# Kernel tuning notes

Hardware: AMD Instinct MI355X
Metric: run time of the kernel (lower is better)

## Reference

```python
import jax, jax.numpy as jnp
import numpy as np

L2 = 65536          # edges per orientation (L=256 torus)
N = 2 * L2          # total edges
FIN = 8             # nfeatCNN_in
FOUT = 8            # nfeatCNN_out
K = 13              # kernel size (neighbor shifts per edge)
SCALE = (2.0 + 2.0 * np.e) / (np.e - 1.0)


def setup_inputs() -> dict:
    key = jax.random.key(0)
    ks = jax.random.split(key, 8)
    x = jax.random.normal(ks[0], (FIN * N,), dtype=jnp.float32)
    Wconv_hor = jax.random.normal(ks[1], (FOUT, FIN, K), dtype=jnp.float32) * 0.1
    Wconv_vert = jax.random.normal(ks[2], (FOUT, FIN, K), dtype=jnp.float32) * 0.1
    bconv_hor = jnp.zeros((FOUT,), dtype=jnp.float32)
    bconv_vert = jnp.zeros((FOUT,), dtype=jnp.float32)
    mask_hor = jax.random.randint(ks[3], (L2, FOUT, FIN, K), 0, 2).astype(bool)
    mask_vert = jax.random.randint(ks[4], (L2, FOUT, FIN, K), 0, 2).astype(bool)
    ker_hor = jax.random.randint(ks[5], (L2, K), 0, N, dtype=jnp.int32)
    ker_vert = jax.random.randint(ks[6], (L2, K), 0, N, dtype=jnp.int32)
    hor_edge_lst = jnp.arange(L2, dtype=jnp.int32)
    vert_edge_lst = jnp.arange(L2, dtype=jnp.int32) + L2
    return {
        "x": x,
        "Wconv_hor": Wconv_hor, "Wconv_vert": Wconv_vert,
        "bconv_hor": bconv_hor, "bconv_vert": bconv_vert,
        "mask_hor": mask_hor, "mask_vert": mask_vert,
        "ker_hor": ker_hor, "ker_vert": ker_vert,
        "hor_edge_lst": hor_edge_lst, "vert_edge_lst": vert_edge_lst,
    }


def reference(x, Wconv_hor, Wconv_vert, bconv_hor, bconv_vert,
              mask_hor, mask_vert, ker_hor, ker_vert,
              hor_edge_lst, vert_edge_lst):
    fout, fin, _ = Wconv_hor.shape
    n = x.shape[0] // fin
    xm = x.reshape(fin, n)                      # (fin, N)

    def branch(W, mask, ker, b):
        xg = xm[:, ker]                         # gather -> (fin, E, K)
        Wm = W[None] * mask.astype(W.dtype)     # (E, fout, fin, K)
        # per-edge masked contraction over (fin, K); vectorized over edges
        z = jnp.einsum('eoik,iek->oe', Wm, xg)  # (fout, E)
        return z + b[:, None]

    x_hor = branch(Wconv_hor, mask_hor, ker_hor, bconv_hor)
    x_vert = branch(Wconv_vert, mask_vert, ker_vert, bconv_vert)

    out = jnp.zeros((fout, n), dtype=x.dtype)
    out = out.at[:, hor_edge_lst].set(x_hor)
    out = out.at[:, vert_edge_lst].set(x_vert)
    return (jax.nn.sigmoid(out) - 0.5) * jnp.asarray(SCALE, out.dtype)
```

## Files before the change

### kernel.cpp

```cpp
#include <hip/hip_runtime.h>
#include <math.h>

#define L2C   65536
#define NC    (2 * L2C)
#define FINC  8
#define FOUTC 8
#define KC    13
#define BLOCK 256
#define EPB   4
#define EWORDS (FOUTC * FINC * KC)

constexpr double E_D = 2.71828182845904523536;
constexpr float SCALE_F = (float)((2.0 + 2.0 * E_D) / (E_D - 1.0));


__global__ __launch_bounds__(256)
void transpose_x_kernel(const float* __restrict__ x, float* __restrict__ xt) {
    int n = blockIdx.x * 256 + threadIdx.x;
    float v[FINC];
#pragma unroll
    for (int i = 0; i < FINC; ++i) v[i] = x[(size_t)i * NC + n];
    float4* dst = reinterpret_cast<float4*>(xt + ((size_t)n << 3));
    dst[0] = make_float4(v[0], v[1], v[2], v[3]);
    dst[1] = make_float4(v[4], v[5], v[6], v[7]);
}

__global__ __launch_bounds__(BLOCK)
void edge_conv_kernel(const float* __restrict__ xt,
                      const float* __restrict__ Wh, const float* __restrict__ Wv,
                      const float* __restrict__ bh, const float* __restrict__ bv,
                      const unsigned char* __restrict__ mh,
                      const unsigned char* __restrict__ mv,
                      const int* __restrict__ kh, const int* __restrict__ kv,
                      float* __restrict__ out)
{
    __shared__ float        Wsh[EWORDS];
    __shared__ unsigned int msh[EPB * EWORDS];

    const int tid  = threadIdx.x;
    const int lane = tid & 63;
    const int wave = tid >> 6;
    const int o    = lane >> 3;
    const int i    = lane & 7;

    const int blk = blockIdx.x;
    const int blocks_per_branch = L2C / EPB;
    const bool hor = (blk < blocks_per_branch);

    const float*         W    = hor ? Wh  : Wv;
    const float*         bias = hor ? bh  : bv;
    const unsigned char* mask = hor ? mh  : mv;
    const int*           ker  = hor ? kh  : kv;
    const int bblk = hor ? blk : blk - blocks_per_branch;
    const int be   = bblk * EPB + wave;
    const int col  = hor ? be : (be + L2C);

    int cols[KC];
#pragma unroll
    for (int k = 0; k < KC; ++k) cols[k] = ker[(size_t)be * KC + k];

    const unsigned char probe = mh[(size_t)(lane * 4 + 1)];
    const bool words = (__ballot(probe != 0) == 0ull);

    if (words) {
        const uint4* g4 = reinterpret_cast<const uint4*>(
            mask + (size_t)bblk * (EPB * EWORDS * 4));
        uint4* m4 = reinterpret_cast<uint4*>(msh);
#pragma unroll
        for (int idx = tid; idx < EPB * EWORDS / 4; idx += BLOCK)
            m4[idx] = g4[idx];
    } else {
        const uint4* g4 = reinterpret_cast<const uint4*>(
            mask + (size_t)bblk * (EPB * EWORDS));
        uint4* m4 = reinterpret_cast<uint4*>(msh);
        if (tid < EPB * EWORDS / 16)
            m4[tid] = g4[tid];
    }

    if (tid < EWORDS / 4)
        reinterpret_cast<float4*>(Wsh)[tid] = reinterpret_cast<const float4*>(W)[tid];

    __syncthreads();

    float acc0 = 0.0f, acc1 = 0.0f;
    if (words) {
        const unsigned int* mrow = msh + wave * EWORDS + lane * KC;
#pragma unroll
        for (int k = 0; k < KC; ++k) {
            const float xv = xt[((size_t)cols[k] << 3) + i];
            const float wk = Wsh[lane * KC + k];
            const float wm = mrow[k] ? wk : 0.0f;
            if (k & 1) acc1 = fmaf(wm, xv, acc1);
            else       acc0 = fmaf(wm, xv, acc0);
        }
    } else {
        const unsigned char* mrow = reinterpret_cast<const unsigned char*>(msh)
                                    + wave * EWORDS + lane * KC;
#pragma unroll
        for (int k = 0; k < KC; ++k) {
            const float xv = xt[((size_t)cols[k] << 3) + i];
            const float wk = Wsh[lane * KC + k];
            const float wm = mrow[k] ? wk : 0.0f;
            if (k & 1) acc1 = fmaf(wm, xv, acc1);
            else       acc0 = fmaf(wm, xv, acc0);
        }
    }
    float acc = acc0 + acc1;

    acc += __shfl_xor(acc, 1);
    acc += __shfl_xor(acc, 2);
    acc += __shfl_xor(acc, 4);

    if (i == 0) {
        const float z   = acc + bias[o];
        const float sig = 1.0f / (1.0f + __expf(-z));
        out[(size_t)o * NC + col] = (sig - 0.5f) * SCALE_F;
    }
}

extern "C" void kernel_launch(void* const* d_in, const int* in_sizes, int n_in,
                              void* d_out, int out_size, void* d_ws, size_t ws_size,
                              hipStream_t stream) {
    const float*         x   = (const float*)d_in[0];
    const float*         Wh  = (const float*)d_in[1];
    const float*         Wv  = (const float*)d_in[2];
    const float*         bh  = (const float*)d_in[3];
    const float*         bv  = (const float*)d_in[4];
    const unsigned char* mh  = (const unsigned char*)d_in[5];
    const unsigned char* mv  = (const unsigned char*)d_in[6];
    const int*           kh  = (const int*)d_in[7];
    const int*           kv  = (const int*)d_in[8];
    float* out = (float*)d_out;
    float* xt  = (float*)d_ws;

    transpose_x_kernel<<<NC / 256, 256, 0, stream>>>(x, xt);
    edge_conv_kernel<<<NC / EPB, BLOCK, 0, stream>>>(
        xt, Wh, Wv, bh, bv, mh, mv, kh, kv, out);
}
```

Before: 458.7 us.

## Make edge-conv blocks persistent over tiles with register-prefetched mask loads

The edge convolution kernel now launches a fixed grid of 2048 blocks. Each block walks 16 consecutive four-edge tiles and prefetches the next tile's mask into registers while the current tile computes. Outputs are staged in shared memory so that each feature row gets one float4 store per tile instead of scattered scalar stores. The weights and bias are loaded once per block. In exchange, every tile now needs two block-wide barriers, and the occupancy hint of 8 may limit registers.

```diff
diff --git a/kernel.cpp b/kernel.cpp
--- a/kernel.cpp
+++ b/kernel.cpp
@@ -9,6 +9,10 @@
 #define BLOCK 256
 #define EPB   4
 #define EWORDS (FOUTC * FINC * KC)
+#define TILE_WBYTES (EPB * EWORDS * 4)
+#define TILE_BBYTES (EPB * EWORDS)
+#define GRID   2048
+#define TILES_PER_BLOCK 16
 
 constexpr double E_D = 2.71828182845904523536;
 constexpr float SCALE_F = (float)((2.0 + 2.0 * E_D) / (E_D - 1.0));
@@ -25,7 +29,7 @@
     dst[1] = make_float4(v[4], v[5], v[6], v[7]);
 }
 
-__global__ __launch_bounds__(BLOCK)
+__global__ __launch_bounds__(BLOCK, 8)
 void edge_conv_kernel(const float* __restrict__ xt,
                       const float* __restrict__ Wh, const float* __restrict__ Wv,
                       const float* __restrict__ bh, const float* __restrict__ bv,
@@ -36,6 +40,7 @@
 {
     __shared__ float        Wsh[EWORDS];
     __shared__ unsigned int msh[EPB * EWORDS];
+    __shared__ float        osh[FOUTC][EPB];
 
     const int tid  = threadIdx.x;
     const int lane = tid & 63;
@@ -43,78 +48,112 @@
     const int o    = lane >> 3;
     const int i    = lane & 7;
 
-    const int blk = blockIdx.x;
-    const int blocks_per_branch = L2C / EPB;
-    const bool hor = (blk < blocks_per_branch);
+    const int  b   = blockIdx.x;
+    const bool hor = (b < GRID / 2);
+    const int  lb  = (hor ? b : b - GRID / 2) * TILES_PER_BLOCK;
 
     const float*         W    = hor ? Wh  : Wv;
     const float*         bias = hor ? bh  : bv;
     const unsigned char* mask = hor ? mh  : mv;
     const int*           ker  = hor ? kh  : kv;
-    const int bblk = hor ? blk : blk - blocks_per_branch;
-    const int be   = bblk * EPB + wave;
-    const int col  = hor ? be : (be + L2C);
-
-    int cols[KC];
-#pragma unroll
-    for (int k = 0; k < KC; ++k) cols[k] = ker[(size_t)be * KC + k];
 
     const unsigned char probe = mh[(size_t)(lane * 4 + 1)];
     const bool words = (__ballot(probe != 0) == 0ull);
 
-    if (words) {
-        const uint4* g4 = reinterpret_cast<const uint4*>(
-            mask + (size_t)bblk * (EPB * EWORDS * 4));
-        uint4* m4 = reinterpret_cast<uint4*>(msh);
-#pragma unroll
-        for (int idx = tid; idx < EPB * EWORDS / 4; idx += BLOCK)
-            m4[idx] = g4[idx];
-    } else {
-        const uint4* g4 = reinterpret_cast<const uint4*>(
-            mask + (size_t)bblk * (EPB * EWORDS));
-        uint4* m4 = reinterpret_cast<uint4*>(msh);
-        if (tid < EPB * EWORDS / 16)
-            m4[tid] = g4[tid];
-    }
-
     if (tid < EWORDS / 4)
         reinterpret_cast<float4*>(Wsh)[tid] = reinterpret_cast<const float4*>(W)[tid];
+    const float biaso = bias[o];
 
+    uint4 r0, r1, r2, r3;
+
+    if (words) {
+        const uint4* g4 = reinterpret_cast<const uint4*>(mask + (size_t)lb * TILE_WBYTES);
+        r0 = g4[tid]; r1 = g4[tid + 256]; r2 = g4[tid + 512];
+        if (tid < 64) r3 = g4[tid + 768];
+        uint4* m4 = reinterpret_cast<uint4*>(msh);
+        m4[tid] = r0; m4[tid + 256] = r1; m4[tid + 512] = r2;
+        if (tid < 64) m4[tid + 768] = r3;
+    } else {
+        const uint4* g4 = reinterpret_cast<const uint4*>(mask + (size_t)lb * TILE_BBYTES);
+        if (tid < 208) {
+            r0 = g4[tid];
+            reinterpret_cast<uint4*>(msh)[tid] = r0;
+        }
+    }
     __syncthreads();
 
-    float acc0 = 0.0f, acc1 = 0.0f;
-    if (words) {
-        const unsigned int* mrow = msh + wave * EWORDS + lane * KC;
+    for (int it = 0; it < TILES_PER_BLOCK; ++it) {
+        const int bblk = lb + it;
+
+        if (it + 1 < TILES_PER_BLOCK) {
+            if (words) {
+                const uint4* g4 = reinterpret_cast<const uint4*>(
+                    mask + (size_t)(bblk + 1) * TILE_WBYTES);
+                r0 = g4[tid]; r1 = g4[tid + 256]; r2 = g4[tid + 512];
+                if (tid < 64) r3 = g4[tid + 768];
+            } else {
+                const uint4* g4 = reinterpret_cast<const uint4*>(
+                    mask + (size_t)(bblk + 1) * TILE_BBYTES);
+                if (tid < 208) r0 = g4[tid];
+            }
+        }
+
+        const int be = bblk * EPB + wave;
+        int cols[KC];
 #pragma unroll
-        for (int k = 0; k < KC; ++k) {
-            const float xv = xt[((size_t)cols[k] << 3) + i];
-            const float wk = Wsh[lane * KC + k];
-            const float wm = mrow[k] ? wk : 0.0f;
-            if (k & 1) acc1 = fmaf(wm, xv, acc1);
-            else       acc0 = fmaf(wm, xv, acc0);
+        for (int k = 0; k < KC; ++k) cols[k] = ker[(size_t)be * KC + k];
+
+        float acc0 = 0.0f, acc1 = 0.0f;
+        if (words) {
+            const unsigned int* mrow = msh + wave * EWORDS + lane * KC;
+#pragma unroll
+            for (int k = 0; k < KC; ++k) {
+                const float xv = xt[((size_t)cols[k] << 3) + i];
+                const float wk = Wsh[lane * KC + k];
+                const float wm = mrow[k] ? wk : 0.0f;
+                if (k & 1) acc1 = fmaf(wm, xv, acc1);
+                else       acc0 = fmaf(wm, xv, acc0);
+            }
+        } else {
+            const unsigned char* mrow = reinterpret_cast<const unsigned char*>(msh)
+                                        + wave * EWORDS + lane * KC;
+#pragma unroll
+            for (int k = 0; k < KC; ++k) {
+                const float xv = xt[((size_t)cols[k] << 3) + i];
+                const float wk = Wsh[lane * KC + k];
+                const float wm = mrow[k] ? wk : 0.0f;
+                if (k & 1) acc1 = fmaf(wm, xv, acc1);
+                else       acc0 = fmaf(wm, xv, acc0);
+            }
         }
-    } else {
-        const unsigned char* mrow = reinterpret_cast<const unsigned char*>(msh)
-                                    + wave * EWORDS + lane * KC;
-#pragma unroll
-        for (int k = 0; k < KC; ++k) {
-            const float xv = xt[((size_t)cols[k] << 3) + i];
-            const float wk = Wsh[lane * KC + k];
-            const float wm = mrow[k] ? wk : 0.0f;
-            if (k & 1) acc1 = fmaf(wm, xv, acc1);
-            else       acc0 = fmaf(wm, xv, acc0);
+        float acc = acc0 + acc1;
+        acc += __shfl_xor(acc, 1);
+        acc += __shfl_xor(acc, 2);
+        acc += __shfl_xor(acc, 4);
+        if (i == 0) {
+            const float z   = acc + biaso;
+            const float sig = 1.0f / (1.0f + __expf(-z));
+            osh[o][wave] = (sig - 0.5f) * SCALE_F;
         }
-    }
-    float acc = acc0 + acc1;
 
-    acc += __shfl_xor(acc, 1);
-    acc += __shfl_xor(acc, 2);
-    acc += __shfl_xor(acc, 4);
+        __syncthreads();
 
-    if (i == 0) {
-        const float z   = acc + bias[o];
-        const float sig = 1.0f / (1.0f + __expf(-z));
-        out[(size_t)o * NC + col] = (sig - 0.5f) * SCALE_F;
+        if (tid < FOUTC) {
+            const int colbase = (hor ? 0 : L2C) + bblk * EPB;
+            *reinterpret_cast<float4*>(out + (size_t)tid * NC + colbase) =
+                *reinterpret_cast<const float4*>(&osh[tid][0]);
+        }
+
+        if (it + 1 < TILES_PER_BLOCK) {
+            if (words) {
+                uint4* m4 = reinterpret_cast<uint4*>(msh);
+                m4[tid] = r0; m4[tid + 256] = r1; m4[tid + 512] = r2;
+                if (tid < 64) m4[tid + 768] = r3;
+            } else {
+                if (tid < 208) reinterpret_cast<uint4*>(msh)[tid] = r0;
+            }
+        }
+        __syncthreads();
     }
 }
 
@@ -134,6 +173,6 @@
     float* xt  = (float*)d_ws;
 
     transpose_x_kernel<<<NC / 256, 256, 0, stream>>>(x, xt);
-    edge_conv_kernel<<<NC / EPB, BLOCK, 0, stream>>>(
+    edge_conv_kernel<<<GRID, BLOCK, 0, stream>>>(
         xt, Wh, Wv, bh, bv, mh, mv, kh, kv, out);
 }
```

New measurement: 547.7 us. 19.4% more time.

## Make edge conv persistent with double-buffered async mask loads into LDS

Applied to the files above, without the earlier changes.

Replaces the one-block-per-4-edges grid with a persistent grid of 1536 blocks that loop over tiles. The mask tile for the next step is prefetched into a second LDS buffer with global_load_lds while the current tile is computed. Weights are kept in registers instead of LDS, and a launch-bounds occupancy hint is added. The aim is to hide mask-load latency and cut per-block setup cost, at the price of a block-wide barrier every iteration and reliance on the asynchronous LDS load ordering.

```diff
diff --git a/kernel.cpp b/kernel.cpp
--- a/kernel.cpp
+++ b/kernel.cpp
@@ -9,10 +9,23 @@
 #define BLOCK 256
 #define EPB   4
 #define EWORDS (FOUTC * FINC * KC)
+#define TILE_WORDS (EPB * EWORDS)
+#define TILE_WBYTES (TILE_WORDS * 4)
+#define TILE_BBYTES (EPB * EWORDS)
+#define GRID  1536
+#define GRIDH (GRID / 2)
+#define TPBR  (L2C / EPB)
 
 constexpr double E_D = 2.71828182845904523536;
 constexpr float SCALE_F = (float)((2.0 + 2.0 * E_D) / (E_D - 1.0));
 
+typedef unsigned int u32;
+typedef __attribute__((address_space(1))) const u32 gu32;
+typedef __attribute__((address_space(3))) u32 lu32;
+
+__device__ __forceinline__ void gll16(const void* g, u32* l) {
+    __builtin_amdgcn_global_load_lds((gu32*)g, (lu32*)l, 16, 0, 0);
+}
 
 __global__ __launch_bounds__(256)
 void transpose_x_kernel(const float* __restrict__ x, float* __restrict__ xt) {
@@ -25,7 +38,7 @@
     dst[1] = make_float4(v[4], v[5], v[6], v[7]);
 }
 
-__global__ __launch_bounds__(BLOCK)
+__global__ __launch_bounds__(BLOCK, 6)
 void edge_conv_kernel(const float* __restrict__ xt,
                       const float* __restrict__ Wh, const float* __restrict__ Wv,
                       const float* __restrict__ bh, const float* __restrict__ bv,
@@ -34,8 +47,7 @@
                       const int* __restrict__ kh, const int* __restrict__ kv,
                       float* __restrict__ out)
 {
-    __shared__ float        Wsh[EWORDS];
-    __shared__ unsigned int msh[EPB * EWORDS];
+    __shared__ __align__(16) u32 msh[2][TILE_WORDS];
 
     const int tid  = threadIdx.x;
     const int lane = tid & 63;
@@ -43,78 +55,92 @@
     const int o    = lane >> 3;
     const int i    = lane & 7;
 
-    const int blk = blockIdx.x;
-    const int blocks_per_branch = L2C / EPB;
-    const bool hor = (blk < blocks_per_branch);
+    const int  b     = blockIdx.x;
+    const bool hor   = (b < GRIDH);
+    const int  bb    = hor ? b : b - GRIDH;
+    const int  cbase = hor ? 0 : L2C;
 
-    const float*         W    = hor ? Wh  : Wv;
-    const float*         bias = hor ? bh  : bv;
-    const unsigned char* mask = hor ? mh  : mv;
-    const int*           ker  = hor ? kh  : kv;
-    const int bblk = hor ? blk : blk - blocks_per_branch;
-    const int be   = bblk * EPB + wave;
-    const int col  = hor ? be : (be + L2C);
-
-    int cols[KC];
-#pragma unroll
-    for (int k = 0; k < KC; ++k) cols[k] = ker[(size_t)be * KC + k];
+    const float*         W    = hor ? Wh : Wv;
+    const float*         bias = hor ? bh : bv;
+    const unsigned char* mask = hor ? mh : mv;
+    const int*           ker  = hor ? kh : kv;
 
     const unsigned char probe = mh[(size_t)(lane * 4 + 1)];
     const bool words = (__ballot(probe != 0) == 0ull);
 
-    if (words) {
-        const uint4* g4 = reinterpret_cast<const uint4*>(
-            mask + (size_t)bblk * (EPB * EWORDS * 4));
-        uint4* m4 = reinterpret_cast<uint4*>(msh);
+    float wreg[KC];
 #pragma unroll
-        for (int idx = tid; idx < EPB * EWORDS / 4; idx += BLOCK)
-            m4[idx] = g4[idx];
-    } else {
-        const uint4* g4 = reinterpret_cast<const uint4*>(
-            mask + (size_t)bblk * (EPB * EWORDS));
-        uint4* m4 = reinterpret_cast<uint4*>(msh);
-        if (tid < EPB * EWORDS / 16)
-            m4[tid] = g4[tid];
-    }
+    for (int k = 0; k < KC; ++k) wreg[k] = W[lane * KC + k];
+    const float biaso = bias[o];
 
-    if (tid < EWORDS / 4)
-        reinterpret_cast<float4*>(Wsh)[tid] = reinterpret_cast<const float4*>(W)[tid];
+    auto stage = [&](int buf, int t) {
+        if (words) {
+            const char* g = (const char*)mask + (size_t)t * TILE_WBYTES;
+#pragma unroll
+            for (int j = 0; j < 3; ++j) {
+                const int c = wave + 4 * j;
+                gll16(g + (size_t)(c * 64 + lane) * 16, &msh[buf][c * 256]);
+            }
+            if (wave == 0)
+                gll16(g + (size_t)(12 * 64 + lane) * 16, &msh[buf][12 * 256]);
+        } else {
+            const char* g = (const char*)mask + (size_t)t * TILE_BBYTES;
+            if (wave < 3)
+                gll16(g + (size_t)(wave * 64 + lane) * 16, &msh[buf][wave * 256]);
+            else if (lane < 16)
+                gll16(g + (size_t)(3 * 64 + lane) * 16, &msh[buf][3 * 256]);
+        }
+    };
 
+    int t = bb;
+    stage(0, t);
     __syncthreads();
 
-    float acc0 = 0.0f, acc1 = 0.0f;
-    if (words) {
-        const unsigned int* mrow = msh + wave * EWORDS + lane * KC;
+    int buf = 0;
+    for (; t < TPBR; t += GRIDH, buf ^= 1) {
+        const int tn = t + GRIDH;
+        if (tn < TPBR) stage(buf ^ 1, tn);
+
+        const int be  = t * EPB + wave;
+        const int bes = __builtin_amdgcn_readfirstlane(be);
+
+        int cols[KC];
 #pragma unroll
-        for (int k = 0; k < KC; ++k) {
-            const float xv = xt[((size_t)cols[k] << 3) + i];
-            const float wk = Wsh[lane * KC + k];
-            const float wm = mrow[k] ? wk : 0.0f;
-            if (k & 1) acc1 = fmaf(wm, xv, acc1);
-            else       acc0 = fmaf(wm, xv, acc0);
+        for (int k = 0; k < KC; ++k) cols[k] = ker[(size_t)bes * KC + k];
+
+        float acc0 = 0.0f, acc1 = 0.0f;
+        if (words) {
+            const u32* mrow = &msh[buf][wave * EWORDS + lane * KC];
+#pragma unroll
+            for (int k = 0; k < KC; ++k) {
+                const float xv = xt[((size_t)cols[k] << 3) + i];
+                const float wm = mrow[k] ? wreg[k] : 0.0f;
+                if (k & 1) acc1 = fmaf(wm, xv, acc1);
+                else       acc0 = fmaf(wm, xv, acc0);
+            }
+        } else {
+            const unsigned char* mrow = (const unsigned char*)&msh[buf][0]
+                                        + wave * EWORDS + lane * KC;
+#pragma unroll
+            for (int k = 0; k < KC; ++k) {
+                const float xv = xt[((size_t)cols[k] << 3) + i];
+                const float wm = mrow[k] ? wreg[k] : 0.0f;
+                if (k & 1) acc1 = fmaf(wm, xv, acc1);
+                else       acc0 = fmaf(wm, xv, acc0);
+            }
         }
-    } else {
-        const unsigned char* mrow = reinterpret_cast<const unsigned char*>(msh)
-                                    + wave * EWORDS + lane * KC;
-#pragma unroll
-        for (int k = 0; k < KC; ++k) {
-            const float xv = xt[((size_t)cols[k] << 3) + i];
-            const float wk = Wsh[lane * KC + k];
-            const float wm = mrow[k] ? wk : 0.0f;
-            if (k & 1) acc1 = fmaf(wm, xv, acc1);
-            else       acc0 = fmaf(wm, xv, acc0);
+        float acc = acc0 + acc1;
+        acc += __shfl_xor(acc, 1);
+        acc += __shfl_xor(acc, 2);
+        acc += __shfl_xor(acc, 4);
+        const float z = acc + biaso;
+
+        __syncthreads();
+
+        if (i == 0) {
+            const float sig = 1.0f / (1.0f + __expf(-z));
+            out[(size_t)o * NC + (cbase + be)] = (sig - 0.5f) * SCALE_F;
         }
-    }
-    float acc = acc0 + acc1;
-
-    acc += __shfl_xor(acc, 1);
-    acc += __shfl_xor(acc, 2);
-    acc += __shfl_xor(acc, 4);
-
-    if (i == 0) {
-        const float z   = acc + bias[o];
-        const float sig = 1.0f / (1.0f + __expf(-z));
-        out[(size_t)o * NC + col] = (sig - 0.5f) * SCALE_F;
     }
 }
 
@@ -134,6 +160,6 @@
     float* xt  = (float*)d_ws;
 
     transpose_x_kernel<<<NC / 256, 256, 0, stream>>>(x, xt);
-    edge_conv_kernel<<<NC / EPB, BLOCK, 0, stream>>>(
+    edge_conv_kernel<<<GRID, BLOCK, 0, stream>>>(
         xt, Wh, Wv, bh, bv, mh, mv, kh, kv, out);
 }
```

Result: no change. 455.2 us (-0.8%).
